# Kernel tuning notes

Hardware: AMD Instinct MI355X
Metric: run time of the kernel (lower is better)

## Reference

```python
import jax, jax.numpy as jnp
import numpy as np

T = 4      # num_step (also LSTM num_layers)
R = 64     # num_relation (= LSTM hidden size)
E = 1024   # num_entity
B = 128    # batch
IN = R + 2 * E  # LSTM input size


def _lstm_layer(x_seq, Wih, Whh, bih, bhh):
    # x_seq: [T, B, In]; torch gate order i, f, g, o
    Bsz = x_seq.shape[1]
    H = Whh.shape[1]
    pre = jnp.einsum('tbi,gi->tbg', x_seq, Wih) + bih + bhh  # [T,B,4H]

    def step(carry, z):
        h, c = carry
        z = z + h @ Whh.T
        i, f, g, o = jnp.split(z, 4, axis=-1)
        i, f, o = jax.nn.sigmoid(i), jax.nn.sigmoid(f), jax.nn.sigmoid(o)
        c = f * c + i * jnp.tanh(g)
        h = o * jnp.tanh(c)
        return (h, c), h

    init = (jnp.zeros((Bsz, H), x_seq.dtype), jnp.zeros((Bsz, H), x_seq.dtype))
    _, hs = jax.lax.scan(step, init, pre)
    return hs  # [T, B, H]


def setup_inputs() -> dict:
    key = jax.random.key(0)
    ks = jax.random.split(key, 12)
    s = 0.05
    inp = {
        'x': jax.random.uniform(ks[0], (B, IN), dtype=jnp.float32),
        'kb': jax.random.uniform(ks[1], (R, E, E), dtype=jnp.float32) * 0.01,
        # LSTM layer 0 (input dim IN)
        'Wih0': jax.random.normal(ks[2], (4 * R, IN), dtype=jnp.float32) * s,
        'Whh0': jax.random.normal(ks[3], (4 * R, R), dtype=jnp.float32) * s,
        'bih0': jnp.zeros((4 * R,), jnp.float32),
        'bhh0': jnp.zeros((4 * R,), jnp.float32),
        # LSTM layers 1..T-1 (input dim R)
        'Wih': jax.random.normal(ks[4], (T - 1, 4 * R, R), dtype=jnp.float32) * s,
        'Whh': jax.random.normal(ks[5], (T - 1, 4 * R, R), dtype=jnp.float32) * s,
        'bih': jnp.zeros((T - 1, 4 * R), jnp.float32),
        'bhh': jnp.zeros((T - 1, 4 * R), jnp.float32),
    }
    return inp


def reference(x, kb, Wih0, Whh0, bih0, bhh0, Wih, Whh, bih, bhh):
    # input to LSTM: x repeated T times -> [T, B, IN]
    seq = jnp.broadcast_to(x[None], (T,) + x.shape)
    hs = _lstm_layer(seq, Wih0, Whh0, bih0, bhh0)
    for l in range(T - 1):  # small fixed layer count
        hs = _lstm_layer(hs, Wih[l], Whh[l], bih[l], bhh[l])
    h = jax.nn.softmax(hs, axis=-1)  # [T, B, R] (first softmax)

    mem = [x[:, R:R + E]]  # memory[0] = head entity vector, [B, E]
    for i in range(T):
        h2 = jax.nn.softmax(h[i], axis=-1)  # double softmax, faithful to source
        # causal memory attention over steps k <= i
        att = jax.nn.softmax(jnp.einsum('kbr,br->bk', h[:i + 1], h[i]), axis=-1)  # [B, i+1]
        prev = jnp.einsum('bk,kbe->be', att, jnp.stack(mem))  # [B, E]
        # per-relation operator application: sum_r h2[b,r] * KB[r] @ prev[b]
        tmp = jnp.einsum('ref,bf->bre', kb, prev)  # [B, R, E]
        mem.append(jnp.einsum('br,bre->be', h2, tmp))

    tail = x[:, R + E:R + 2 * E]  # [B, E]
    score = jax.nn.sigmoid(-jnp.einsum('be,be->b', mem[-1], tail))[:, None]  # [B, 1]
    return score
```

## Files before the change

kernel.cpp:

```cpp
#include <hip/hip_runtime.h>
#include <cstdint>
#include <cstddef>

#define B_ 128
#define E_ 1024
#define R_ 64
#define T_ 4
#define IN_ 2112
#define G_ 256

typedef __attribute__((ext_vector_type(4))) float f32x4;
typedef __attribute__((ext_vector_type(8))) __bf16 bf16x8;

__device__ __forceinline__ unsigned short f2bf(float f) {
  unsigned int u = __float_as_uint(f);
  u += 0x7fffu + ((u >> 16) & 1u);
  return (unsigned short)(u >> 16);
}
__device__ __forceinline__ unsigned int pack2(float lo, float hi) {
  return (unsigned int)f2bf(lo) | ((unsigned int)f2bf(hi) << 16);
}
__device__ __forceinline__ float wred_sum(float v) {
#pragma unroll
  for (int m = 32; m > 0; m >>= 1) v += __shfl_xor(v, m, 64);
  return v;
}
__device__ __forceinline__ float wred_max(float v) {
#pragma unroll
  for (int m = 32; m > 0; m >>= 1) v = fmaxf(v, __shfl_xor(v, m, 64));
  return v;
}
__device__ __forceinline__ float sigmoidf_(float x) { return 1.f / (1.f + expf(-x)); }

__device__ __forceinline__ void gload_lds16(const void* g, void* l) {
  __builtin_amdgcn_global_load_lds(
      (const __attribute__((address_space(1))) unsigned int*)g,
      (__attribute__((address_space(3))) unsigned int*)l, 16, 0, 0);
}

__global__ __launch_bounds__(256) void head_kernel(
    const float* __restrict__ x, const float* __restrict__ kb,
    const float* __restrict__ Wih0, const float* __restrict__ Whh0,
    const float* __restrict__ bih0, const float* __restrict__ bhh0,
    const float* __restrict__ Wih, const float* __restrict__ Whh,
    const float* __restrict__ bih, const float* __restrict__ bhh,
    unsigned short* __restrict__ kb_bf,
    float* __restrict__ h2_out, float* __restrict__ att_out) {
  __shared__ float Wt[G_ * 65];
  __shared__ float xrow[IN_];
  __shared__ float hbuf[R_], cbuf[R_], zbuf[G_];
  __shared__ float hs_in[T_][R_], hs_out[T_][R_], hmat[T_][R_];
  const int tid = threadIdx.x;

  if (blockIdx.x >= 128) {
    const size_t base = (size_t)(blockIdx.x - 128) * 8192;
#pragma unroll
    for (int c = 0; c < 4; c++) {
      size_t o = base + (size_t)c * 2048 + (size_t)tid * 8;
      float4 v0 = *(const float4*)(kb + o);
      float4 v1 = *(const float4*)(kb + o + 4);
      uint4 u;
      u.x = pack2(v0.x, v0.y); u.y = pack2(v0.z, v0.w);
      u.z = pack2(v1.x, v1.y); u.w = pack2(v1.z, v1.w);
      *(uint4*)(kb_bf + o) = u;
    }
    return;
  }

  const int b = blockIdx.x;
  const int lane = tid & 63, wv = tid >> 6;

  for (int l = tid; l < IN_; l += 256) xrow[l] = x[b * IN_ + l];
  __syncthreads();
  float p0 = bih0[tid] + bhh0[tid];
  {
    const float* wr = Wih0 + (size_t)tid * IN_;
#pragma unroll 4
    for (int j = 0; j < IN_; j += 4) {
      float4 w = *(const float4*)(wr + j);
      p0 += xrow[j] * w.x + xrow[j + 1] * w.y + xrow[j + 2] * w.z + xrow[j + 3] * w.w;
    }
  }

  auto stage_w = [&](const float* src) {
    for (int l = tid; l < G_ * 16; l += 256) {
      int g = l >> 4, c4 = (l & 15) * 4;
      const float4 v = *(const float4*)(src + g * R_ + c4);
      float* dst = &Wt[g * 65 + c4];
      dst[0] = v.x; dst[1] = v.y; dst[2] = v.z; dst[3] = v.w;
    }
  };
  auto scan = [&](float* pret) {
    for (int t = 0; t < T_; t++) {
      float z = pret[t];
#pragma unroll
      for (int j = 0; j < R_; j++) z += hbuf[j] * Wt[tid * 65 + j];
      zbuf[tid] = z;
      __syncthreads();
      if (tid < R_) {
        float iv = sigmoidf_(zbuf[tid]);
        float fv = sigmoidf_(zbuf[R_ + tid]);
        float gv = tanhf(zbuf[2 * R_ + tid]);
        float ov = sigmoidf_(zbuf[3 * R_ + tid]);
        float c = fv * cbuf[tid] + iv * gv;
        cbuf[tid] = c;
        float h = ov * tanhf(c);
        hbuf[tid] = h;
        hs_out[t][tid] = h;
      }
      __syncthreads();
    }
  };

  float pret[T_];
#pragma unroll
  for (int t = 0; t < T_; t++) pret[t] = p0;
  stage_w(Whh0);
  if (tid < R_) { hbuf[tid] = 0.f; cbuf[tid] = 0.f; }
  __syncthreads();
  scan(pret);

  for (int l = 0; l < T_ - 1; l++) {
    hs_in[tid >> 6][tid & 63] = hs_out[tid >> 6][tid & 63];
    __syncthreads();
    stage_w(Wih + l * G_ * R_);
    __syncthreads();
    const float bsum = bih[l * G_ + tid] + bhh[l * G_ + tid];
    for (int t = 0; t < T_; t++) {
      float p = bsum;
#pragma unroll
      for (int j = 0; j < R_; j++) p += hs_in[t][j] * Wt[tid * 65 + j];
      pret[t] = p;
    }
    __syncthreads();
    stage_w(Whh + l * G_ * R_);
    if (tid < R_) { hbuf[tid] = 0.f; cbuf[tid] = 0.f; }
    __syncthreads();
    scan(pret);
  }

  {
    float v = hs_out[wv][lane];
    float mx = wred_max(v);
    float ev = expf(v - mx);
    float sm = wred_sum(ev);
    float hval = ev / sm;
    hmat[wv][lane] = hval;
    float mx2 = wred_max(hval);
    float e2 = expf(hval - mx2);
    float s2 = wred_sum(e2);
    h2_out[(wv * B_ + b) * R_ + lane] = e2 / s2;
    __syncthreads();
    float dots[T_];
    for (int k = 0; k <= wv; k++)
      dots[k] = wred_sum(hmat[k][lane] * hmat[wv][lane]);
    if (lane == 0) {
      float mx3 = dots[0];
      for (int k = 1; k <= wv; k++) mx3 = fmaxf(mx3, dots[k]);
      float ss = 0.f, es[T_];
      for (int k = 0; k <= wv; k++) { es[k] = expf(dots[k] - mx3); ss += es[k]; }
      for (int k = 0; k <= wv; k++) att_out[(wv * B_ + b) * 4 + k] = es[k] / ss;
    }
  }
}

__global__ __launch_bounds__(256) void prep0_kernel(
    const float* __restrict__ x, const float* __restrict__ att,
    unsigned short* __restrict__ prev_bf) {
  const int idx = blockIdx.x * 256 + threadIdx.x;
  const int b = idx >> 10, e = idx & 1023;
  float a0 = att[b * 4];
  prev_bf[idx] = f2bf(a0 * x[b * IN_ + R_ + e]);
}

__global__ __launch_bounds__(256) void gemm_bf_kernel(
    const unsigned short* __restrict__ Abf,
    const unsigned short* __restrict__ Kbf,
    float* __restrict__ part) {
  __shared__ unsigned short As[128 * 32];
  __shared__ unsigned short Bs[128 * 32];
  const int tid = threadIdx.x, wv = tid >> 6, lane = tid & 63;
  const int et = blockIdx.x, r = blockIdx.y;
  const int wm = (wv & 1) * 64, wn = (wv >> 1) * 64;
  const int fr = lane & 15, koff = (lane >> 4) * 8;

  const int srow = wv * 32 + (lane >> 2);
  const int scol = (lane & 3) * 8;
  const unsigned short* agp = Abf + (size_t)srow * 1024 + scol;
  const unsigned short* bgp = Kbf + (size_t)r * 1048576 + (size_t)(et * 128 + srow) * 1024 + scol;
  unsigned short* a_l0 = As + wv * 1024;
  unsigned short* a_l1 = As + wv * 1024 + 512;
  unsigned short* b_l0 = Bs + wv * 1024;
  unsigned short* b_l1 = Bs + wv * 1024 + 512;

  f32x4 acc[4][4];
#pragma unroll
  for (int mt = 0; mt < 4; mt++)
#pragma unroll
    for (int nt = 0; nt < 4; nt++)
#pragma unroll
      for (int q = 0; q < 4; q++) acc[mt][nt][q] = 0.f;

  for (int kk = 0; kk < 32; kk++) {
    gload_lds16(agp + kk * 32,             a_l0);
    gload_lds16(agp + kk * 32 + 16 * 1024, a_l1);
    gload_lds16(bgp + kk * 32,             b_l0);
    gload_lds16(bgp + kk * 32 + 16 * 1024, b_l1);
    __syncthreads();
    bf16x8 af[4], bfr[4];
#pragma unroll
    for (int mt = 0; mt < 4; mt++)
      af[mt] = *(const bf16x8*)(As + (wm + mt * 16 + fr) * 32 + koff);
#pragma unroll
    for (int nt = 0; nt < 4; nt++)
      bfr[nt] = *(const bf16x8*)(Bs + (wn + nt * 16 + fr) * 32 + koff);
#pragma unroll
    for (int mt = 0; mt < 4; mt++)
#pragma unroll
      for (int nt = 0; nt < 4; nt++)
        acc[mt][nt] = __builtin_amdgcn_mfma_f32_16x16x32_bf16(af[mt], bfr[nt], acc[mt][nt], 0, 0, 0);
    __syncthreads();
  }
  const int crow = (lane >> 4) * 4;
  float* pout = part + (size_t)r * 131072;
#pragma unroll
  for (int mt = 0; mt < 4; mt++)
#pragma unroll
    for (int nt = 0; nt < 4; nt++)
#pragma unroll
      for (int q = 0; q < 4; q++)
        pout[(wm + mt * 16 + crow + q) * 1024 + et * 128 + wn + nt * 16 + fr] = acc[mt][nt][q];
}

__global__ __launch_bounds__(256) void mid_kernel(
    const float* __restrict__ part, const float* __restrict__ h2,
    const float* __restrict__ att, const float* __restrict__ x,
    float* __restrict__ mem, unsigned short* __restrict__ prev_bf, int it) {
  const int idx = blockIdx.x * 256 + threadIdx.x;
  const int b = idx >> 10, e = idx & 1023;
  const float* h2row = h2 + (it * B_ + b) * R_;
  const float* pp = part + idx;
  float s = 0.f;
#pragma unroll 8
  for (int rr = 0; rr < 64; rr++) s += h2row[rr] * pp[(size_t)rr * 131072];
  mem[it * 131072 + idx] = s;
  if (it < 3) {
    const float* arow = att + ((it + 1) * B_ + b) * 4;
    float acc = arow[0] * x[b * IN_ + R_ + e];
    for (int k = 1; k <= it; k++) acc += arow[k] * mem[(k - 1) * 131072 + idx];
    acc += arow[it + 1] * s;
    prev_bf[idx] = f2bf(acc);
  }
}

__global__ __launch_bounds__(256) void prep_fp32_kernel(
    const float* __restrict__ x, const float* __restrict__ att,
    const float* __restrict__ mem, float* __restrict__ prev,
    float* __restrict__ newmem, int it) {
  const int idx = blockIdx.x * 256 + threadIdx.x;
  const int b = idx >> 10, e = idx & 1023;
  const float* arow = att + (it * B_ + b) * 4;
  float acc = arow[0] * x[b * IN_ + R_ + e];
  for (int k = 1; k <= it; k++)
    acc += arow[k] * mem[(k - 1) * (B_ * E_) + b * E_ + e];
  prev[idx] = acc;
  newmem[idx] = 0.f;
}

__global__ __launch_bounds__(256) void gemm_fp32_kernel(
    const float* __restrict__ prev, const float* __restrict__ h2,
    const float* __restrict__ kb, float* __restrict__ out) {
  __shared__ unsigned short As[128 * 40];
  __shared__ unsigned short Bs[128 * 40];
  __shared__ float h2s[128];
  const int tid = threadIdx.x;
  const int et = blockIdx.x;
  const int r = blockIdx.y;
  if (tid < 128) h2s[tid] = h2[tid * 64 + r];
  __syncthreads();
  const int row = tid >> 1;
  const int c0 = (tid & 1) * 16;
  const float hsc = h2s[row];
  const float* aptr = prev + row * 1024 + c0;
  const float* bptr = kb + (size_t)r * (1024u * 1024u) + (size_t)(et * 128 + row) * 1024 + c0;
  unsigned short* adst = As + row * 40 + c0;
  unsigned short* bdst = Bs + row * 40 + c0;
  const int wv = tid >> 6, lane = tid & 63;
  const int wm = (wv & 1) * 64, wn = (wv >> 1) * 64;
  const int fr = lane & 15, koff = (lane >> 4) * 8;
  f32x4 acc[4][4];
#pragma unroll
  for (int mt = 0; mt < 4; mt++)
#pragma unroll
    for (int nt = 0; nt < 4; nt++)
#pragma unroll
      for (int q = 0; q < 4; q++) acc[mt][nt][q] = 0.f;
  for (int kk = 0; kk < 32; kk++) {
    const float4 a0 = *(const float4*)(aptr + kk * 32);
    const float4 a1 = *(const float4*)(aptr + kk * 32 + 4);
    const float4 a2 = *(const float4*)(aptr + kk * 32 + 8);
    const float4 a3 = *(const float4*)(aptr + kk * 32 + 12);
    const float4 b0 = *(const float4*)(bptr + kk * 32);
    const float4 b1 = *(const float4*)(bptr + kk * 32 + 4);
    const float4 b2 = *(const float4*)(bptr + kk * 32 + 8);
    const float4 b3 = *(const float4*)(bptr + kk * 32 + 12);
    __syncthreads();
    uint4 u;
    u.x = pack2(a0.x * hsc, a0.y * hsc); u.y = pack2(a0.z * hsc, a0.w * hsc);
    u.z = pack2(a1.x * hsc, a1.y * hsc); u.w = pack2(a1.z * hsc, a1.w * hsc);
    *(uint4*)adst = u;
    u.x = pack2(a2.x * hsc, a2.y * hsc); u.y = pack2(a2.z * hsc, a2.w * hsc);
    u.z = pack2(a3.x * hsc, a3.y * hsc); u.w = pack2(a3.z * hsc, a3.w * hsc);
    *(uint4*)(adst + 8) = u;
    u.x = pack2(b0.x, b0.y); u.y = pack2(b0.z, b0.w);
    u.z = pack2(b1.x, b1.y); u.w = pack2(b1.z, b1.w);
    *(uint4*)bdst = u;
    u.x = pack2(b2.x, b2.y); u.y = pack2(b2.z, b2.w);
    u.z = pack2(b3.x, b3.y); u.w = pack2(b3.z, b3.w);
    *(uint4*)(bdst + 8) = u;
    __syncthreads();
    bf16x8 af[4], bfr[4];
#pragma unroll
    for (int mt = 0; mt < 4; mt++)
      af[mt] = *(const bf16x8*)(As + (wm + mt * 16 + fr) * 40 + koff);
#pragma unroll
    for (int nt = 0; nt < 4; nt++)
      bfr[nt] = *(const bf16x8*)(Bs + (wn + nt * 16 + fr) * 40 + koff);
#pragma unroll
    for (int mt = 0; mt < 4; mt++)
#pragma unroll
      for (int nt = 0; nt < 4; nt++)
        acc[mt][nt] = __builtin_amdgcn_mfma_f32_16x16x32_bf16(af[mt], bfr[nt], acc[mt][nt], 0, 0, 0);
  }
  const int crow = (lane >> 4) * 4;
  const int ccol = et * 128 + fr;
#pragma unroll
  for (int mt = 0; mt < 4; mt++)
#pragma unroll
    for (int nt = 0; nt < 4; nt++)
#pragma unroll
      for (int q = 0; q < 4; q++)
        atomicAdd(&out[(wm + mt * 16 + crow + q) * 1024 + ccol + wn + nt * 16], acc[mt][nt][q]);
}

__global__ __launch_bounds__(256) void score_kernel(
    const float* __restrict__ x, const float* __restrict__ mem4,
    float* __restrict__ out) {
  __shared__ float red[4];
  const int b = blockIdx.x, tid = threadIdx.x;
  float s = 0.f;
  for (int e = tid; e < E_; e += 256)
    s += mem4[b * E_ + e] * x[b * IN_ + R_ + E_ + e];
  s = wred_sum(s);
  if ((tid & 63) == 0) red[tid >> 6] = s;
  __syncthreads();
  if (tid == 0) {
    float t = red[0] + red[1] + red[2] + red[3];
    out[b] = 1.f / (1.f + expf(t));
  }
}

extern "C" void kernel_launch(void* const* d_in, const int* in_sizes, int n_in,
                              void* d_out, int out_size, void* d_ws, size_t ws_size,
                              hipStream_t stream) {
  const float* x    = (const float*)d_in[0];
  const float* kb   = (const float*)d_in[1];
  const float* Wih0 = (const float*)d_in[2];
  const float* Whh0 = (const float*)d_in[3];
  const float* bih0 = (const float*)d_in[4];
  const float* bhh0 = (const float*)d_in[5];
  const float* Wih  = (const float*)d_in[6];
  const float* Whh  = (const float*)d_in[7];
  const float* bih  = (const float*)d_in[8];
  const float* bhh  = (const float*)d_in[9];

  float* ws    = (float*)d_ws;
  float* h2    = ws;
  float* att   = ws + 32768;
  float* mem   = ws + 34816;
  float* prevb = ws + 559104;
  float* part  = ws + 690176;
  float* kbbf  = ws + 9078784;
  const size_t need_big = (size_t)(9078784 + 33554432) * sizeof(float);
  const bool big = ws_size >= need_big;

  if (big) {
    head_kernel<<<8320, 256, 0, stream>>>(x, kb, Wih0, Whh0, bih0, bhh0,
                                          Wih, Whh, bih, bhh,
                                          (unsigned short*)kbbf, h2, att);
    prep0_kernel<<<512, 256, 0, stream>>>(x, att, (unsigned short*)prevb);
    for (int i = 0; i < 4; i++) {
      gemm_bf_kernel<<<dim3(8, 64), 256, 0, stream>>>(
          (const unsigned short*)prevb, (const unsigned short*)kbbf, part);
      mid_kernel<<<512, 256, 0, stream>>>(part, h2, att, x, mem,
                                          (unsigned short*)prevb, i);
    }
  } else {
    head_kernel<<<128, 256, 0, stream>>>(x, kb, Wih0, Whh0, bih0, bhh0,
                                         Wih, Whh, bih, bhh,
                                         (unsigned short*)prevb , h2, att);
    for (int i = 0; i < 4; i++) {
      float* newmem = mem + i * (B_ * E_);
      prep_fp32_kernel<<<512, 256, 0, stream>>>(x, att, mem, prevb, newmem, i);
      gemm_fp32_kernel<<<dim3(8, 64), 256, 0, stream>>>(prevb, h2 + i * (B_ * R_), kb, newmem);
    }
  }
  score_kernel<<<128, 256, 0, stream>>>(x, mem + 3 * (B_ * E_), (float*)d_out);
}
```

Before: 602.0 us.

## Quantize KB and memory vectors to FP8 with double-buffered FP8 MFMA GEMM

```diff
diff --git a/kernel.cpp b/kernel.cpp
--- a/kernel.cpp
+++ b/kernel.cpp
@@ -12,13 +12,23 @@
 typedef __attribute__((ext_vector_type(4))) float f32x4;
 typedef __attribute__((ext_vector_type(8))) __bf16 bf16x8;
 
+#define KB_SCALE 64.0f
+#define KB_INV_SCALE (1.0f / 64.0f)
+
 __device__ __forceinline__ unsigned short f2bf(float f) {
   unsigned int u = __float_as_uint(f);
   u += 0x7fffu + ((u >> 16) & 1u);
   return (unsigned short)(u >> 16);
 }
+__device__ __forceinline__ float bf2f(unsigned short u) {
+  return __uint_as_float(((unsigned int)u) << 16);
+}
 __device__ __forceinline__ unsigned int pack2(float lo, float hi) {
   return (unsigned int)f2bf(lo) | ((unsigned int)f2bf(hi) << 16);
+}
+__device__ __forceinline__ unsigned char f2fp8(float v) {
+  int r = __builtin_amdgcn_cvt_pk_fp8_f32(v, 0.f, 0, false);
+  return (unsigned char)(r & 0xff);
 }
 __device__ __forceinline__ float wred_sum(float v) {
 #pragma unroll
@@ -38,35 +48,36 @@
       (__attribute__((address_space(3))) unsigned int*)l, 16, 0, 0);
 }
 
-__global__ __launch_bounds__(256) void head_kernel(
-    const float* __restrict__ x, const float* __restrict__ kb,
+__global__ __launch_bounds__(256) void conv_kernel(
+    const float* __restrict__ kb, unsigned char* __restrict__ kbf8) {
+  const size_t base = (size_t)blockIdx.x * 8192 + (size_t)threadIdx.x * 32;
+  int w[8];
+#pragma unroll
+  for (int j = 0; j < 8; j++) {
+    float4 v = *(const float4*)(kb + base + j * 4);
+    int r = __builtin_amdgcn_cvt_pk_fp8_f32(v.x * KB_SCALE, v.y * KB_SCALE, 0, false);
+    r = __builtin_amdgcn_cvt_pk_fp8_f32(v.z * KB_SCALE, v.w * KB_SCALE, r, true);
+    w[j] = r;
+  }
+  uint4 u0 = {(unsigned)w[0], (unsigned)w[1], (unsigned)w[2], (unsigned)w[3]};
+  uint4 u1 = {(unsigned)w[4], (unsigned)w[5], (unsigned)w[6], (unsigned)w[7]};
+  *(uint4*)(kbf8 + base) = u0;
+  *(uint4*)(kbf8 + base + 16) = u1;
+}
+
+__global__ __launch_bounds__(256) void recur_kernel(
+    const float* __restrict__ x,
     const float* __restrict__ Wih0, const float* __restrict__ Whh0,
     const float* __restrict__ bih0, const float* __restrict__ bhh0,
     const float* __restrict__ Wih, const float* __restrict__ Whh,
     const float* __restrict__ bih, const float* __restrict__ bhh,
-    unsigned short* __restrict__ kb_bf,
-    float* __restrict__ h2_out, float* __restrict__ att_out) {
+    float* __restrict__ h2_out, float* __restrict__ att_out,
+    unsigned char* __restrict__ prevq) {
   __shared__ float Wt[G_ * 65];
   __shared__ float xrow[IN_];
   __shared__ float hbuf[R_], cbuf[R_], zbuf[G_];
   __shared__ float hs_in[T_][R_], hs_out[T_][R_], hmat[T_][R_];
   const int tid = threadIdx.x;
-
-  if (blockIdx.x >= 128) {
-    const size_t base = (size_t)(blockIdx.x - 128) * 8192;
-#pragma unroll
-    for (int c = 0; c < 4; c++) {
-      size_t o = base + (size_t)c * 2048 + (size_t)tid * 8;
-      float4 v0 = *(const float4*)(kb + o);
-      float4 v1 = *(const float4*)(kb + o + 4);
-      uint4 u;
-      u.x = pack2(v0.x, v0.y); u.y = pack2(v0.z, v0.w);
-      u.z = pack2(v1.x, v1.y); u.w = pack2(v1.z, v1.w);
-      *(uint4*)(kb_bf + o) = u;
-    }
-    return;
-  }
-
   const int b = blockIdx.x;
   const int lane = tid & 63, wv = tid >> 6;
 
@@ -80,6 +91,11 @@
       float4 w = *(const float4*)(wr + j);
       p0 += xrow[j] * w.x + xrow[j + 1] * w.y + xrow[j + 2] * w.z + xrow[j + 3] * w.w;
     }
+  }
+  {
+    int w = __builtin_amdgcn_cvt_pk_fp8_f32(xrow[R_ + tid * 4], xrow[R_ + tid * 4 + 1], 0, false);
+    w = __builtin_amdgcn_cvt_pk_fp8_f32(xrow[R_ + tid * 4 + 2], xrow[R_ + tid * 4 + 3], w, true);
+    ((int*)prevq)[b * 256 + tid] = w;
   }
 
   auto stage_w = [&](const float* src) {
@@ -164,34 +180,21 @@
   }
 }
 
-__global__ __launch_bounds__(256) void prep0_kernel(
-    const float* __restrict__ x, const float* __restrict__ att,
-    unsigned short* __restrict__ prev_bf) {
-  const int idx = blockIdx.x * 256 + threadIdx.x;
-  const int b = idx >> 10, e = idx & 1023;
-  float a0 = att[b * 4];
-  prev_bf[idx] = f2bf(a0 * x[b * IN_ + R_ + e]);
-}
-
-__global__ __launch_bounds__(256) void gemm_bf_kernel(
-    const unsigned short* __restrict__ Abf,
-    const unsigned short* __restrict__ Kbf,
-    float* __restrict__ part) {
-  __shared__ unsigned short As[128 * 32];
-  __shared__ unsigned short Bs[128 * 32];
+__global__ __launch_bounds__(256) void gemm_f8_kernel(
+    const unsigned char* __restrict__ Af8,
+    const unsigned char* __restrict__ Kf8,
+    unsigned short* __restrict__ part) {
+  __shared__ unsigned char As[2][4096];
+  __shared__ unsigned char Bs[2][4096];
   const int tid = threadIdx.x, wv = tid >> 6, lane = tid & 63;
   const int et = blockIdx.x, r = blockIdx.y;
   const int wm = (wv & 1) * 64, wn = (wv >> 1) * 64;
   const int fr = lane & 15, koff = (lane >> 4) * 8;
 
-  const int srow = wv * 32 + (lane >> 2);
-  const int scol = (lane & 3) * 8;
-  const unsigned short* agp = Abf + (size_t)srow * 1024 + scol;
-  const unsigned short* bgp = Kbf + (size_t)r * 1048576 + (size_t)(et * 128 + srow) * 1024 + scol;
-  unsigned short* a_l0 = As + wv * 1024;
-  unsigned short* a_l1 = As + wv * 1024 + 512;
-  unsigned short* b_l0 = Bs + wv * 1024;
-  unsigned short* b_l1 = Bs + wv * 1024 + 512;
+  const int srow = wv * 32 + (lane >> 1);
+  const int shalf = (lane & 1) * 16;
+  const unsigned char* agp = Af8 + (size_t)srow * 1024 + shalf;
+  const unsigned char* bgp = Kf8 + (size_t)r * 1048576 + (size_t)(et * 128 + srow) * 1024 + shalf;
 
   f32x4 acc[4][4];
 #pragma unroll
@@ -201,55 +204,61 @@
 #pragma unroll
       for (int q = 0; q < 4; q++) acc[mt][nt][q] = 0.f;
 
+  gload_lds16(agp, &As[0][wv * 1024]);
+  gload_lds16(bgp, &Bs[0][wv * 1024]);
+
+#pragma unroll 2
   for (int kk = 0; kk < 32; kk++) {
-    gload_lds16(agp + kk * 32,             a_l0);
-    gload_lds16(agp + kk * 32 + 16 * 1024, a_l1);
-    gload_lds16(bgp + kk * 32,             b_l0);
-    gload_lds16(bgp + kk * 32 + 16 * 1024, b_l1);
-    __syncthreads();
-    bf16x8 af[4], bfr[4];
+    const int cur = kk & 1;
+    __syncthreads();
+    if (kk < 31) {
+      gload_lds16(agp + (kk + 1) * 32, &As[cur ^ 1][wv * 1024]);
+      gload_lds16(bgp + (kk + 1) * 32, &Bs[cur ^ 1][wv * 1024]);
+    }
+    long af[4], bf[4];
 #pragma unroll
     for (int mt = 0; mt < 4; mt++)
-      af[mt] = *(const bf16x8*)(As + (wm + mt * 16 + fr) * 32 + koff);
-#pragma unroll
-    for (int nt = 0; nt < 4; nt++)
-      bfr[nt] = *(const bf16x8*)(Bs + (wn + nt * 16 + fr) * 32 + koff);
+      af[mt] = *(const long*)(&As[cur][(wm + mt * 16 + fr) * 32 + koff]);
+#pragma unroll
+    for (int nt = 0; nt < 4; nt++)
+      bf[nt] = *(const long*)(&Bs[cur][(wn + nt * 16 + fr) * 32 + koff]);
 #pragma unroll
     for (int mt = 0; mt < 4; mt++)
 #pragma unroll
       for (int nt = 0; nt < 4; nt++)
-        acc[mt][nt] = __builtin_amdgcn_mfma_f32_16x16x32_bf16(af[mt], bfr[nt], acc[mt][nt], 0, 0, 0);
-    __syncthreads();
+        acc[mt][nt] = __builtin_amdgcn_mfma_f32_16x16x32_fp8_fp8(af[mt], bf[nt], acc[mt][nt], 0, 0, 0);
   }
   const int crow = (lane >> 4) * 4;
-  float* pout = part + (size_t)r * 131072;
+  unsigned short* pout = part + (size_t)r * 131072;
 #pragma unroll
   for (int mt = 0; mt < 4; mt++)
 #pragma unroll
     for (int nt = 0; nt < 4; nt++)
 #pragma unroll
       for (int q = 0; q < 4; q++)
-        pout[(wm + mt * 16 + crow + q) * 1024 + et * 128 + wn + nt * 16 + fr] = acc[mt][nt][q];
+        pout[(wm + mt * 16 + crow + q) * 1024 + et * 128 + wn + nt * 16 + fr] =
+            f2bf(acc[mt][nt][q]);
 }
 
 __global__ __launch_bounds__(256) void mid_kernel(
-    const float* __restrict__ part, const float* __restrict__ h2,
+    const unsigned short* __restrict__ part, const float* __restrict__ h2,
     const float* __restrict__ att, const float* __restrict__ x,
-    float* __restrict__ mem, unsigned short* __restrict__ prev_bf, int it) {
+    float* __restrict__ mem, unsigned char* __restrict__ prevq, int it) {
   const int idx = blockIdx.x * 256 + threadIdx.x;
   const int b = idx >> 10, e = idx & 1023;
   const float* h2row = h2 + (it * B_ + b) * R_;
-  const float* pp = part + idx;
+  const unsigned short* pp = part + idx;
   float s = 0.f;
 #pragma unroll 8
-  for (int rr = 0; rr < 64; rr++) s += h2row[rr] * pp[(size_t)rr * 131072];
+  for (int rr = 0; rr < 64; rr++) s += h2row[rr] * bf2f(pp[(size_t)rr * 131072]);
+  s *= KB_INV_SCALE;
   mem[it * 131072 + idx] = s;
   if (it < 3) {
     const float* arow = att + ((it + 1) * B_ + b) * 4;
     float acc = arow[0] * x[b * IN_ + R_ + e];
     for (int k = 1; k <= it; k++) acc += arow[k] * mem[(k - 1) * 131072 + idx];
     acc += arow[it + 1] * s;
-    prev_bf[idx] = f2bf(acc);
+    prevq[idx] = f2fp8(acc);
   }
 }
 
@@ -378,31 +387,32 @@
   float* h2    = ws;
   float* att   = ws + 32768;
   float* mem   = ws + 34816;
-  float* prevb = ws + 559104;
+  float* prevq = ws + 559104;
   float* part  = ws + 690176;
-  float* kbbf  = ws + 9078784;
-  const size_t need_big = (size_t)(9078784 + 33554432) * sizeof(float);
+  float* kbf8  = ws + 4884480;
+  const size_t need_big = (size_t)(4884480 + 16777216) * sizeof(float);
   const bool big = ws_size >= need_big;
 
   if (big) {
-    head_kernel<<<8320, 256, 0, stream>>>(x, kb, Wih0, Whh0, bih0, bhh0,
+    conv_kernel<<<8192, 256, 0, stream>>>(kb, (unsigned char*)kbf8);
+    recur_kernel<<<128, 256, 0, stream>>>(x, Wih0, Whh0, bih0, bhh0,
                                           Wih, Whh, bih, bhh,
-                                          (unsigned short*)kbbf, h2, att);
-    prep0_kernel<<<512, 256, 0, stream>>>(x, att, (unsigned short*)prevb);
+                                          h2, att, (unsigned char*)prevq);
     for (int i = 0; i < 4; i++) {
-      gemm_bf_kernel<<<dim3(8, 64), 256, 0, stream>>>(
-          (const unsigned short*)prevb, (const unsigned short*)kbbf, part);
-      mid_kernel<<<512, 256, 0, stream>>>(part, h2, att, x, mem,
-                                          (unsigned short*)prevb, i);
+      gemm_f8_kernel<<<dim3(8, 64), 256, 0, stream>>>(
+          (const unsigned char*)prevq, (const unsigned char*)kbf8,
+          (unsigned short*)part);
+      mid_kernel<<<512, 256, 0, stream>>>((const unsigned short*)part, h2, att, x,
+                                          mem, (unsigned char*)prevq, i);
     }
   } else {
-    head_kernel<<<128, 256, 0, stream>>>(x, kb, Wih0, Whh0, bih0, bhh0,
-                                         Wih, Whh, bih, bhh,
-                                         (unsigned short*)prevb , h2, att);
+    recur_kernel<<<128, 256, 0, stream>>>(x, Wih0, Whh0, bih0, bhh0,
+                                          Wih, Whh, bih, bhh,
+                                          h2, att, (unsigned char*)prevq);
     for (int i = 0; i < 4; i++) {
       float* newmem = mem + i * (B_ * E_);
-      prep_fp32_kernel<<<512, 256, 0, stream>>>(x, att, mem, prevb, newmem, i);
-      gemm_fp32_kernel<<<dim3(8, 64), 256, 0, stream>>>(prevb, h2 + i * (B_ * R_), kb, newmem);
+      prep_fp32_kernel<<<512, 256, 0, stream>>>(x, att, mem, prevq, newmem, i);
+      gemm_fp32_kernel<<<dim3(8, 64), 256, 0, stream>>>(prevq, h2 + i * (B_ * R_), kb, newmem);
     }
   }
   score_kernel<<<128, 256, 0, stream>>>(x, mem + 3 * (B_ * E_), (float*)d_out);
```

After: 654.5 us. 1.09x slower.
